# Kernel optimization log

Hardware: AMD Instinct MI355X
Metric: run time of the kernel (lower is better)

Reference implementation:

```python
import jax, jax.numpy as jnp
import numpy as np

# Model dims (see init_kwargs)
B, S, D = 2, 2048, 2048          # batch, seq, hidden
H, HD = 16, 128                  # heads, head_dim (= ND + RD)
ND, RD = 64, 64                  # nope dim, rope dim per head
R = 512                          # kv lora rank
THETA = 10000.0


def _rotate_half(x):
    # interleaved rotation: pairs (x0,x1) -> (-x1, x0)
    x1 = x[..., ::2]
    x2 = x[..., 1::2]
    return jnp.stack((-x2, x1), axis=-1).reshape(x.shape)


def apply_rope(x, positions):
    # x: [..., seq, dim]
    dim = x.shape[-1]
    freqs = 1.0 / THETA ** (jnp.arange(0, dim, 2, dtype=x.dtype) / dim)  # [dim/2]
    angles = positions.astype(x.dtype)[:, None] * freqs                  # [seq, dim/2]
    cos = jnp.repeat(jnp.cos(angles), 2, axis=-1)[None, None]            # [1,1,seq,dim]
    sin = jnp.repeat(jnp.sin(angles), 2, axis=-1)[None, None]
    return x * cos + _rotate_half(x) * sin


def setup_inputs() -> dict:
    key = jax.random.key(0)
    ks = jax.random.split(key, 7)
    def lin(k, out_f, in_f):  # torch Linear convention: weight [out, in]
        return jax.random.normal(k, (out_f, in_f), dtype=jnp.float32) * (in_f ** -0.5)
    return {
        "x": jax.random.normal(ks[0], (B, S, D), dtype=jnp.float32),
        "wq": lin(ks[1], D, D),
        "w_kv_down": lin(ks[2], R, D),
        "w_k_up": lin(ks[3], H * ND, R),
        "w_k_rope": lin(ks[4], RD, D),
        "w_v_up": lin(ks[5], D, R),
        "wo": lin(ks[6], D, D),
    }


def reference(x, wq, w_kv_down, w_k_up, w_k_rope, w_v_up, wo):
    b, s, _ = x.shape
    pos = jnp.arange(s)
    scale = 1.0 / np.sqrt(HD).astype(np.float32)

    # queries: [b,H,s,HD] split into nope/rope parts, rope applied per head
    q = (x @ wq.T).reshape(b, s, H, HD).transpose(0, 2, 1, 3)
    q_nope = q[..., :ND]
    q_rope = apply_rope(q[..., ND:], pos)

    # compressed kv latent: [b,s,R]
    c_kv = x @ w_kv_down.T
    k_nope = (c_kv @ w_k_up.T).reshape(b, s, H, ND).transpose(0, 2, 1, 3)  # [b,H,s,ND]
    k_rope = apply_rope((x @ w_k_rope.T)[:, None], pos)[:, 0]             # [b,s,RD], shared across heads
    v = (c_kv @ w_v_up.T).reshape(b, s, H, HD).transpose(0, 2, 1, 3)      # [b,H,s,HD]

    # decomposed scores: nope part (per head) + rope part (shared k)
    scores = jnp.einsum('bhqd,bhkd->bhqk', q_nope, k_nope)
    scores = scores + jnp.einsum('bhqd,bkd->bhqk', q_rope, k_rope)
    scores = scores * scale

    causal = jnp.tril(jnp.ones((s, s), dtype=bool))
    scores = jnp.where(causal[None, None], scores, jnp.finfo(scores.dtype).min)
    attn = jax.nn.softmax(scores, axis=-1)

    out = jnp.einsum('bhqk,bhkd->bhqd', attn, v)
    out = out.transpose(0, 2, 1, 3).reshape(b, s, D)
    return out @ wo.T
```

## Files before the change

### kernel.cpp

```cpp
#include <hip/hip_runtime.h>
#include <stdint.h>


typedef unsigned short u16;
typedef __bf16 bf16x8 __attribute__((ext_vector_type(8)));
typedef float f32x4 __attribute__((ext_vector_type(4)));

__device__ __forceinline__ float bf2f(u16 u) {
    union { unsigned int i; float f; } x; x.i = ((unsigned int)u) << 16; return x.f;
}
__device__ __forceinline__ u16 f2bf(float f) {
    union { float f; unsigned int i; } x; x.f = f;
    unsigned int r = x.i + 0x7fffu + ((x.i >> 16) & 1u);
    return (u16)(r >> 16);
}
__device__ __forceinline__ void store_c(u16* p, float v)  { *p = f2bf(v); }
__device__ __forceinline__ void store_c(float* p, float v){ *p = v; }

#define GLOBAL_AS __attribute__((address_space(1)))
#define LDS_AS    __attribute__((address_space(3)))
__device__ __forceinline__ void gl_lds16(const void* g, void* l) {
    __builtin_amdgcn_global_load_lds((GLOBAL_AS const void*)g, (LDS_AS void*)l, 16, 0, 0);
}

template<int CTRL>
__device__ __forceinline__ float fmax_dpp(float v) {
    int s = __builtin_bit_cast(int, v);
    int t = __builtin_amdgcn_update_dpp(s, s, CTRL, 0xF, 0xF, true);
    return fmaxf(v, __builtin_bit_cast(float, t));
}
__device__ __forceinline__ float rowmax16(float v) {
    v = fmax_dpp<0xB1>(v);
    v = fmax_dpp<0x4E>(v);
    v = fmax_dpp<0x124>(v);
    v = fmax_dpp<0x128>(v);
    return v;
}

__global__ void convert_in(const float* __restrict__ src, u16* __restrict__ dst,
                           int n8) {
    int i = blockIdx.x * 256 + threadIdx.x;
    if (i >= n8) return;
    const float4* s = (const float4*)src;
    float4 v0 = s[2*i], v1 = s[2*i + 1];
    union { u16 u[8]; uint4 v; } o;
    o.u[0] = f2bf(v0.x); o.u[1] = f2bf(v0.y); o.u[2] = f2bf(v0.z); o.u[3] = f2bf(v0.w);
    o.u[4] = f2bf(v1.x); o.u[5] = f2bf(v1.y); o.u[6] = f2bf(v1.z); o.u[7] = f2bf(v1.w);
    *((uint4*)(dst + 8*i)) = o.v;
}

template<int BM, int BN, int EPI, typename CT>
__global__ __launch_bounds__((BM/64)*(BN/64)*64)
void gemm_bt(const u16* __restrict__ A, const u16* __restrict__ W,
             CT* __restrict__ C, int M, int N, int K,
             int lda, int ldw, int ldc) {
    constexpr int BK = 32;
    constexpr int NWAVE = (BM/64)*(BN/64);
    constexpr int NT = NWAVE * 64;
    __shared__ u16 As[BM*BK];
    __shared__ u16 Bs[BN*BK];
    const int tid  = threadIdx.x;
    const int lane = tid & 63, l15 = lane & 15, quad = lane >> 4;
    const int wave = tid >> 6;
    const int wm = wave % (BM/64);
    const int wn = wave / (BM/64);
    const int bm = blockIdx.y * BM;
    const int bn = blockIdx.x * BN;

    const f32x4 fzero = {0.f, 0.f, 0.f, 0.f};
    f32x4 acc[4][4];
    #pragma unroll
    for (int i = 0; i < 4; ++i)
        #pragma unroll
        for (int j = 0; j < 4; ++j) acc[i][j] = fzero;

    const size_t Ab = (size_t)lda * 2;
    const size_t Wb = (size_t)ldw * 2;

    for (int k0 = 0; k0 < K; k0 += BK) {
        #pragma unroll
        for (int i = 0; i < (BM*64)/(NT*16); ++i) {
            int o = (tid + i*NT) * 16;
            int row = o >> 6, colb = o & 63;
            gl_lds16((const char*)A + (size_t)(bm + row)*Ab + (size_t)k0*2 + colb,
                     (char*)As + o);
        }
        #pragma unroll
        for (int i = 0; i < (BN*64)/(NT*16); ++i) {
            int o = (tid + i*NT) * 16;
            int row = o >> 6, colb = o & 63;
            gl_lds16((const char*)W + (size_t)(bn + row)*Wb + (size_t)k0*2 + colb,
                     (char*)Bs + o);
        }
        __syncthreads();

        bf16x8 af[4], bfv[4];
        #pragma unroll
        for (int mt = 0; mt < 4; ++mt)
            af[mt] = *reinterpret_cast<const bf16x8*>(&As[(wm*64 + mt*16 + l15)*BK + quad*8]);
        #pragma unroll
        for (int nt = 0; nt < 4; ++nt)
            bfv[nt] = *reinterpret_cast<const bf16x8*>(&Bs[(wn*64 + nt*16 + l15)*BK + quad*8]);
        #pragma unroll
        for (int mt = 0; mt < 4; ++mt)
            #pragma unroll
            for (int nt = 0; nt < 4; ++nt)
                acc[mt][nt] = __builtin_amdgcn_mfma_f32_16x16x32_bf16(
                    af[mt], bfv[nt], acc[mt][nt], 0, 0, 0);
        __syncthreads();
    }

    #pragma unroll
    for (int mt = 0; mt < 4; ++mt)
        #pragma unroll
        for (int nt = 0; nt < 4; ++nt)
            #pragma unroll
            for (int r = 0; r < 4; ++r) {
                int gm = bm + wm*64 + mt*16 + quad*4 + r;
                int gn = bn + wn*64 + nt*16 + l15;
                size_t ci;
                if (EPI == 1) ci = (size_t)gm*ldc + ((gn >> 6)*128 + (gn & 63));
                else          ci = (size_t)gm*ldc + gn;
                store_c(&C[ci], acc[mt][nt][r]);
            }
}

__global__ void rope_q(u16* __restrict__ qcat) {
    int idx = blockIdx.x * 256 + threadIdx.x;
    int i = idx & 31, h = (idx >> 5) & 15, r = idx >> 9;
    int pos = r & 2047;
    float freq = powf(10000.0f, -(float)i * (1.0f/32.0f));
    float ang  = (float)pos * freq;
    float s = sinf(ang), c = cosf(ang);
    u16* p = qcat + (size_t)r * 2688 + h*128 + 64 + 2*i;
    float x0 = bf2f(p[0]), x1 = bf2f(p[1]);
    p[0] = f2bf(x0*c - x1*s);
    p[1] = f2bf(x1*c + x0*s);
}

__global__ void rope_kr_bcast(const u16* __restrict__ qcat, u16* __restrict__ keff) {
    int idx = blockIdx.x * 256 + threadIdx.x;
    int i = idx & 31, r = idx >> 5;
    int pos = r & 2047;
    float freq = powf(10000.0f, -(float)i * (1.0f/32.0f));
    float ang  = (float)pos * freq;
    float s = sinf(ang), c = cosf(ang);
    const u16* p = qcat + (size_t)r * 2688 + 2048 + 2*i;
    float x0 = bf2f(p[0]), x1 = bf2f(p[1]);
    union { u16 u[2]; unsigned int w; } o;
    o.u[0] = f2bf(x0*c - x1*s);
    o.u[1] = f2bf(x1*c + x0*s);
    unsigned int* base = (unsigned int*)(keff + (size_t)r*2048 + 64 + 2*i);
    #pragma unroll
    for (int h = 0; h < 16; ++h) base[h*64] = o.w;
}

__global__ __launch_bounds__(256, 3)
void attn_kernel(u16* __restrict__ qcat, const u16* __restrict__ KE,
                 const u16* __restrict__ VT) {
    constexpr int S = 2048;
    const int bh = blockIdx.y;
    const int b = bh >> 4, h = bh & 15;

    __shared__ u16 Ks[64*128];
    __shared__ u16 Vs[128*64];
    __shared__ u16 Ps[64*68];

    const int tid  = threadIdx.x;
    const int lane = tid & 63, l15 = lane & 15, quad = lane >> 4;
    const int wave = tid >> 6;

    const u16* ksrc[4];
    const u16* vsrc[4];
    #pragma unroll
    for (int i = 0; i < 4; ++i) {
        int g = tid + i*256;
        {
            int r = g >> 4, slot = g & 15, cg = slot ^ (r & 15);
            ksrc[i] = KE + (size_t)(b*S + r)*2048 + h*128 + cg*8;
        }
        {
            int d = g >> 3, slot = g & 7, cg = slot ^ (d & 7);
            vsrc[i] = VT + (size_t)(h*128 + d)*4096 + (size_t)(b*S) + cg*8;
        }
    }

    bf16x8 kreg[4], vreg[4];
    #pragma unroll
    for (int i = 0; i < 4; ++i) {
        kreg[i] = *reinterpret_cast<const bf16x8*>(ksrc[i]);
        vreg[i] = *reinterpret_cast<const bf16x8*>(vsrc[i]);
    }

    union { u16 u[8]; bf16x8 v; } onesu;
    #pragma unroll
    for (int i = 0; i < 8; ++i) onesu.u[i] = 0x3f80;
    const bf16x8 ones = onesu.v;

    const f32x4 fzero = {0.f, 0.f, 0.f, 0.f};
    const float NEG = -1e30f;
    const float scale = 0.08838834764831845f;

    for (int half = 0; half < 2; ++half) {
        const int qt = half ? (int)blockIdx.x : 31 - (int)blockIdx.x;
        const int nkt = qt + 1;

        u16* qbase = qcat + (size_t)(b*S + qt*64) * 2688 + h*128;
        bf16x8 aq[4];
        #pragma unroll
        for (int ks = 0; ks < 4; ++ks)
            aq[ks] = *reinterpret_cast<const bf16x8*>(
                qbase + (size_t)(wave*16 + l15)*2688 + ks*32 + quad*8);

        float m_i[4] = {NEG, NEG, NEG, NEG};
        float l_i[4] = {0.f, 0.f, 0.f, 0.f};
        f32x4 oacc[8];
        #pragma unroll
        for (int i = 0; i < 8; ++i) oacc[i] = fzero;

        const int qrow0 = qt*64 + wave*16 + quad*4;

        for (int kt = 0; kt < nkt; ++kt) {
            #pragma unroll
            for (int i = 0; i < 4; ++i) {
                *reinterpret_cast<bf16x8*>(&Ks[(tid + i*256) * 8]) = kreg[i];
                *reinterpret_cast<bf16x8*>(&Vs[(tid + i*256) * 8]) = vreg[i];
            }
            {
                int ktn = (kt + 1 < nkt) ? kt + 1 : 0;
                #pragma unroll
                for (int i = 0; i < 4; ++i) {
                    kreg[i] = *reinterpret_cast<const bf16x8*>(ksrc[i] + (size_t)ktn*(64*2048));
                    vreg[i] = *reinterpret_cast<const bf16x8*>(vsrc[i] + (size_t)ktn*64);
                }
            }
            __syncthreads();

            f32x4 sfr[4];
            #pragma unroll
            for (int nt = 0; nt < 4; ++nt) {
                f32x4 s = fzero;
                int n = nt*16 + l15;
                #pragma unroll
                for (int ks = 0; ks < 4; ++ks) {
                    int c = ks*4 + quad;
                    bf16x8 bk = *reinterpret_cast<const bf16x8*>(&Ks[n*128 + ((c ^ l15) * 8)]);
                    s = __builtin_amdgcn_mfma_f32_16x16x32_bf16(aq[ks], bk, s, 0, 0, 0);
                }
                sfr[nt] = s;
            }
            #pragma unroll
            for (int nt = 0; nt < 4; ++nt) {
                int kg = kt*64 + nt*16 + l15;
                #pragma unroll
                for (int r = 0; r < 4; ++r) {
                    float v = sfr[nt][r] * scale;
                    sfr[nt][r] = (kg <= qrow0 + r) ? v : NEG;
                }
            }
            float rm[4];
            #pragma unroll
            for (int r = 0; r < 4; ++r) {
                rm[r] = fmaxf(fmaxf(sfr[0][r], sfr[1][r]), fmaxf(sfr[2][r], sfr[3][r]));
                rm[r] = rowmax16(rm[r]);
            }

            float alpha[4];
            #pragma unroll
            for (int r = 0; r < 4; ++r) {
                float mn = fmaxf(m_i[r], rm[r]);
                alpha[r] = __expf(m_i[r] - mn);
                m_i[r] = mn;
                l_i[r] *= alpha[r];
            }
            float pf[4][4];
            #pragma unroll
            for (int nt = 0; nt < 4; ++nt)
                #pragma unroll
                for (int r = 0; r < 4; ++r)
                    pf[nt][r] = __expf(sfr[nt][r] - m_i[r]);
            #pragma unroll
            for (int i = 0; i < 8; ++i)
                #pragma unroll
                for (int r = 0; r < 4; ++r)
                    oacc[i][r] *= alpha[r];

            #pragma unroll
            for (int nt = 0; nt < 4; ++nt)
                #pragma unroll
                for (int r = 0; r < 4; ++r)
                    Ps[(wave*16 + quad*4 + r)*68 + nt*16 + l15] = f2bf(pf[nt][r]);

            f32x4 lfr = fzero;
            #pragma unroll
            for (int ks = 0; ks < 2; ++ks) {
                bf16x8 pa = *reinterpret_cast<const bf16x8*>(
                    &Ps[(wave*16 + l15)*68 + ks*32 + quad*8]);
                lfr = __builtin_amdgcn_mfma_f32_16x16x32_bf16(pa, ones, lfr, 0, 0, 0);
                #pragma unroll
                for (int ntv = 0; ntv < 8; ++ntv) {
                    int c = ks*4 + quad;
                    bf16x8 bv = *reinterpret_cast<const bf16x8*>(
                        &Vs[(ntv*16 + l15)*64 + ((c ^ (l15 & 7)) * 8)]);
                    oacc[ntv] = __builtin_amdgcn_mfma_f32_16x16x32_bf16(pa, bv, oacc[ntv], 0, 0, 0);
                }
            }
            #pragma unroll
            for (int r = 0; r < 4; ++r) l_i[r] += lfr[r];
            __syncthreads();
        }

        #pragma unroll
        for (int r = 0; r < 4; ++r) {
            float inv = 1.0f / l_i[r];
            int qrow = wave*16 + quad*4 + r;
            #pragma unroll
            for (int ntv = 0; ntv < 8; ++ntv) {
                int d = ntv*16 + l15;
                qbase[(size_t)qrow*2688 + d] = f2bf(oacc[ntv][r] * inv);
            }
        }
    }
}

extern "C" void kernel_launch(void* const* d_in, const int* in_sizes, int n_in,
                              void* d_out, int out_size, void* d_ws, size_t ws_size,
                              hipStream_t stream) {
    (void)in_sizes; (void)n_in; (void)out_size; (void)ws_size;
    float* out = (float*)d_out;
    char* ws = (char*)d_ws;

    u16* xc     = (u16*)(ws);
    u16* qcat   = (u16*)(ws + 16777216);
    u16* keff   = (u16*)(ws + 38797312);
    u16* wqcat  = (u16*)(ws + 55574528);
    u16* kupc   = (u16*)(ws + 66584576);
    u16* vupc   = (u16*)(ws + 67633152);
    u16* vT     = xc;
    u16* woc    = wqcat;

    convert_in<<<(1048576+255)/256, 256, 0, stream>>>((const float*)d_in[0], xc, 1048576);
    convert_in<<<( 524288+255)/256, 256, 0, stream>>>((const float*)d_in[1], wqcat, 524288);
    convert_in<<<(  16384+255)/256, 256, 0, stream>>>((const float*)d_in[4], wqcat + 2048*2048, 16384);
    convert_in<<<( 131072+255)/256, 256, 0, stream>>>((const float*)d_in[2], wqcat + 2112*2048, 131072);
    convert_in<<<(  65536+255)/256, 256, 0, stream>>>((const float*)d_in[3], kupc, 65536);
    convert_in<<<( 131072+255)/256, 256, 0, stream>>>((const float*)d_in[5], vupc, 131072);

    gemm_bt<128,128,0><<<dim3(21, 32), 256, 0, stream>>>(
        xc, wqcat, qcat, 4096, 2688, 2048, 2048, 2048, 2688);

    convert_in<<<(524288+255)/256, 256, 0, stream>>>((const float*)d_in[6], woc, 524288);

    rope_q<<<8192, 256, 0, stream>>>(qcat);
    rope_kr_bcast<<<512, 256, 0, stream>>>(qcat, keff);

    gemm_bt<128,128,1><<<dim3(8, 32), 256, 0, stream>>>(
        qcat + 2112, kupc, keff, 4096, 1024, 512, 2688, 512, 2048);

    gemm_bt<128,128,0><<<dim3(32, 16), 256, 0, stream>>>(
        vupc, qcat + 2112, vT, 2048, 4096, 512, 512, 2688, 4096);

    attn_kernel<<<dim3(16, 32), 256, 0, stream>>>(qcat, keff, vT);

    gemm_bt<128,128,0><<<dim3(16, 32), 256, 0, stream>>>(
        qcat, woc, out, 4096, 2048, 2048, 2688, 2048, 2048);
}
```

Baseline: 383.0 us.

## Use exp2 softmax with lazy rescale, mask only diagonal tile, remap blocks to XCDs

The attention softmax now folds scale and log2e into one constant and uses hardware exp2. Rescaling of the output accumulators is skipped unless a row's max grows past a threshold. The causal mask is applied only on the diagonal tile, and P is stored through the native bf16 conversion. Blocks are remapped so each XCD handles a contiguous set of batch-heads for better L2 reuse, and rope_q now does all 16 heads per thread with one sin/cos, using fewer blocks. Lazy rescaling trades exactness for fewer multiplies and bounds growth with a threshold that could risk bf16 overflow.

```diff
diff --git a/kernel.cpp b/kernel.cpp
--- a/kernel.cpp
+++ b/kernel.cpp
@@ -22,6 +22,12 @@
 __device__ __forceinline__ void gl_lds16(const void* g, void* l) {
     __builtin_amdgcn_global_load_lds((GLOBAL_AS const void*)g, (LDS_AS void*)l, 16, 0, 0);
 }
+
+#if __has_builtin(__builtin_amdgcn_exp2f)
+__device__ __forceinline__ float exp2fast(float x) { return __builtin_amdgcn_exp2f(x); }
+#else
+__device__ __forceinline__ float exp2fast(float x) { return __expf(x * 0.6931471805599453f); }
+#endif
 
 template<int CTRL>
 __device__ __forceinline__ float fmax_dpp(float v) {
@@ -127,15 +133,21 @@
 
 __global__ void rope_q(u16* __restrict__ qcat) {
     int idx = blockIdx.x * 256 + threadIdx.x;
-    int i = idx & 31, h = (idx >> 5) & 15, r = idx >> 9;
+    int i = idx & 31, r = idx >> 5;
     int pos = r & 2047;
     float freq = powf(10000.0f, -(float)i * (1.0f/32.0f));
     float ang  = (float)pos * freq;
     float s = sinf(ang), c = cosf(ang);
-    u16* p = qcat + (size_t)r * 2688 + h*128 + 64 + 2*i;
-    float x0 = bf2f(p[0]), x1 = bf2f(p[1]);
-    p[0] = f2bf(x0*c - x1*s);
-    p[1] = f2bf(x1*c + x0*s);
+    u16* row = qcat + (size_t)r * 2688 + 64 + 2*i;
+    #pragma unroll
+    for (int h = 0; h < 16; ++h) {
+        unsigned int* p = (unsigned int*)(row + h*128);
+        unsigned int v = *p;
+        float x0 = bf2f((u16)(v & 0xffffu)), x1 = bf2f((u16)(v >> 16));
+        unsigned int lo = f2bf(x0*c - x1*s);
+        unsigned int hi = f2bf(x1*c + x0*s);
+        *p = lo | (hi << 16);
+    }
 }
 
 __global__ void rope_kr_bcast(const u16* __restrict__ qcat, u16* __restrict__ keff) {
@@ -159,7 +171,10 @@
 void attn_kernel(u16* __restrict__ qcat, const u16* __restrict__ KE,
                  const u16* __restrict__ VT) {
     constexpr int S = 2048;
-    const int bh = blockIdx.y;
+    const int L = (int)blockIdx.y * 16 + (int)blockIdx.x;
+    const int xcd = L & 7, j = L >> 3;
+    const int bh   = xcd * 4 + (j & 3);
+    const int pair = j >> 2;
     const int b = bh >> 4, h = bh & 15;
 
     __shared__ u16 Ks[64*128];
@@ -199,10 +214,13 @@
 
     const f32x4 fzero = {0.f, 0.f, 0.f, 0.f};
     const float NEG = -1e30f;
-    const float scale = 0.08838834764831845f;
+    const float KLOG = 0.12751739f;
+    const float THR = 8.0f;
+
+    __bf16* PsB = reinterpret_cast<__bf16*>(Ps);
 
     for (int half = 0; half < 2; ++half) {
-        const int qt = half ? (int)blockIdx.x : 31 - (int)blockIdx.x;
+        const int qt = half ? pair : 31 - pair;
         const int nkt = qt + 1;
 
         u16* qbase = qcat + (size_t)(b*S + qt*64) * 2688 + h*128;
@@ -212,7 +230,7 @@
             aq[ks] = *reinterpret_cast<const bf16x8*>(
                 qbase + (size_t)(wave*16 + l15)*2688 + ks*32 + quad*8);
 
-        float m_i[4] = {NEG, NEG, NEG, NEG};
+        float m2[4]  = {NEG, NEG, NEG, NEG};
         float l_i[4] = {0.f, 0.f, 0.f, 0.f};
         f32x4 oacc[8];
         #pragma unroll
@@ -221,6 +239,7 @@
         const int qrow0 = qt*64 + wave*16 + quad*4;
 
         for (int kt = 0; kt < nkt; ++kt) {
+            const bool is_last = (kt == nkt - 1);
             #pragma unroll
             for (int i = 0; i < 4; ++i) {
                 *reinterpret_cast<bf16x8*>(&Ks[(tid + i*256) * 8]) = kreg[i];
@@ -249,13 +268,13 @@
                 }
                 sfr[nt] = s;
             }
-            #pragma unroll
-            for (int nt = 0; nt < 4; ++nt) {
-                int kg = kt*64 + nt*16 + l15;
-                #pragma unroll
-                for (int r = 0; r < 4; ++r) {
-                    float v = sfr[nt][r] * scale;
-                    sfr[nt][r] = (kg <= qrow0 + r) ? v : NEG;
+            if (is_last) {
+                #pragma unroll
+                for (int nt = 0; nt < 4; ++nt) {
+                    int kg = kt*64 + nt*16 + l15;
+                    #pragma unroll
+                    for (int r = 0; r < 4; ++r)
+                        if (kg > qrow0 + r) sfr[nt][r] = NEG;
                 }
             }
             float rm[4];
@@ -264,32 +283,42 @@
                 rm[r] = fmaxf(fmaxf(sfr[0][r], sfr[1][r]), fmaxf(sfr[2][r], sfr[3][r]));
                 rm[r] = rowmax16(rm[r]);
             }
-
-            float alpha[4];
+            float c2[4];
+            int need = 0;
             #pragma unroll
             for (int r = 0; r < 4; ++r) {
-                float mn = fmaxf(m_i[r], rm[r]);
-                alpha[r] = __expf(m_i[r] - mn);
-                m_i[r] = mn;
-                l_i[r] *= alpha[r];
+                c2[r] = rm[r] * KLOG;
+                need |= (c2[r] > m2[r] + THR) ? 1 : 0;
+            }
+            if (__any(need)) {
+                float alpha[4];
+                #pragma unroll
+                for (int r = 0; r < 4; ++r) {
+                    float mn = fmaxf(m2[r], c2[r]);
+                    alpha[r] = exp2fast(m2[r] - mn);
+                    m2[r] = mn;
+                    l_i[r] *= alpha[r];
+                }
+                #pragma unroll
+                for (int i = 0; i < 8; ++i)
+                    #pragma unroll
+                    for (int r = 0; r < 4; ++r)
+                        oacc[i][r] *= alpha[r];
             }
             float pf[4][4];
             #pragma unroll
             for (int nt = 0; nt < 4; ++nt)
                 #pragma unroll
                 for (int r = 0; r < 4; ++r)
-                    pf[nt][r] = __expf(sfr[nt][r] - m_i[r]);
-            #pragma unroll
-            for (int i = 0; i < 8; ++i)
+                    pf[nt][r] = exp2fast(__builtin_fmaf(sfr[nt][r], KLOG, -m2[r]));
+
+            #pragma unroll
+            for (int nt = 0; nt < 4; ++nt) {
+                int base = (wave*16 + quad*4)*68 + nt*16 + l15;
                 #pragma unroll
                 for (int r = 0; r < 4; ++r)
-                    oacc[i][r] *= alpha[r];
-
-            #pragma unroll
-            for (int nt = 0; nt < 4; ++nt)
-                #pragma unroll
-                for (int r = 0; r < 4; ++r)
-                    Ps[(wave*16 + quad*4 + r)*68 + nt*16 + l15] = f2bf(pf[nt][r]);
+                    PsB[base + r*68] = (__bf16)pf[nt][r];
+            }
 
             f32x4 lfr = fzero;
             #pragma unroll
@@ -351,7 +380,7 @@
 
     convert_in<<<(524288+255)/256, 256, 0, stream>>>((const float*)d_in[6], woc, 524288);
 
-    rope_q<<<8192, 256, 0, stream>>>(qcat);
+    rope_q<<<512, 256, 0, stream>>>(qcat);
     rope_kr_bcast<<<512, 256, 0, stream>>>(qcat, keff);
 
     gemm_bt<128,128,1><<<dim3(8, 32), 256, 0, stream>>>(
```

Measured after the change: 360.9 us. 1.06x faster.
